# Kernel tuning notes

Measured on AMD Instinct MI355X. Metric: run time of the kernel, lower is better.

Reference implementation:

```python
import jax, jax.numpy as jnp
import numpy as np

B = 2048   # num_trajectories
T = 32     # rollout
I = 1024   # input_size
H = 1024   # hidden_size


def setup_inputs() -> dict:
    key = jax.random.key(0)
    ks = jax.random.split(key, 5)
    head_output = jax.random.normal(ks[0], (B * T, I), jnp.float32)
    rnn_states = jax.random.normal(ks[1], (B, 2 * H), jnp.float32)
    dones = (jax.random.uniform(ks[2], (B * T,)) < 0.05).astype(jnp.float32)
    s = 1.0 / np.sqrt(H)
    w_ih = jax.random.uniform(ks[3], (4 * H, I), jnp.float32, -s, s)
    w_hh = jax.random.uniform(ks[4], (4 * H, H), jnp.float32, -s, s)
    b_ih = jnp.zeros((4 * H,), jnp.float32)  # initialize() fills biases with 0
    b_hh = jnp.zeros((4 * H,), jnp.float32)
    return {"head_output": head_output, "rnn_states": rnn_states, "dones": dones,
            "w_ih": w_ih, "w_hh": w_hh, "b_ih": b_ih, "b_hh": b_hh, "rollout": T}


def reference(head_output, rnn_states, dones, w_ih, w_hh, b_ih, b_hh, rollout):
    # is_seq=True path, n_rnn_layer=1
    n_traj = head_output.shape[0] // rollout
    Hh = rnn_states.shape[1] // 2
    h0, c0 = rnn_states[:, :Hh], rnn_states[:, Hh:]          # [B,H] each
    x = head_output.reshape(n_traj, rollout, -1).transpose(1, 0, 2)  # [T,B,I]
    # is_new_episode = roll(dones, 1, time); first step never resets
    resets = jnp.roll(dones.reshape(n_traj, rollout), 1, axis=1).at[:, 0].set(0.0).T  # [T,B]
    # Precompute the input GEMM for all timesteps in one big matmul
    x_gates = jnp.einsum('tbi,gi->tbg', x, w_ih) + b_ih + b_hh  # [T,B,4H]

    def step(carry, inp):
        h, c = carry
        xg, r = inp
        keep = (1.0 - r)[:, None]
        h = h * keep
        c = c * keep
        gates = xg + h @ w_hh.T                                # [B,4H]
        i, f, g, o = jnp.split(gates, 4, axis=1)               # torch gate order i,f,g,o
        i = jax.nn.sigmoid(i)
        f = jax.nn.sigmoid(f)
        g = jnp.tanh(g)
        o = jax.nn.sigmoid(o)
        c = f * c + i * g
        h = o * jnp.tanh(c)
        return (h, c), h

    (h, c), outs = jax.lax.scan(step, (h0, c0), (x_gates, resets))
    x_out = outs.transpose(1, 0, 2).reshape(n_traj * rollout, -1)  # permute(1,0,2).flatten(0,1)
    new_rnn_states = jnp.concatenate([h, c], axis=1)               # [B,2H]
    return x_out, new_rnn_states
```

## Files before the change

### kernel.cpp

```cpp
#include <hip/hip_runtime.h>
#include <stdint.h>

typedef __attribute__((ext_vector_type(8))) short short8;
typedef __attribute__((ext_vector_type(4))) float f32x4;

#define NTRAJ 2048
#define TSTEP 32
#define HDIM  1024
#define KCAT  2048
#define NGATE 4096

__device__ __forceinline__ unsigned short f2bf(float f) {
  union { float f; unsigned int u; } v; v.f = f;
  unsigned int u = v.u + 0x7FFFu + ((v.u >> 16) & 1u);
  return (unsigned short)(u >> 16);
}
__device__ __forceinline__ float sigmoidf_(float x) {
  return 1.0f / (1.0f + __expf(-x));
}
__device__ __forceinline__ float tanhf_(float x) {
  return 1.0f - 2.0f / (__expf(2.0f * x) + 1.0f);
}

__device__ __forceinline__ void async_lds16(const void* g, void* l) {
  __builtin_amdgcn_global_load_lds(
      (const __attribute__((address_space(1))) unsigned int*)g,
      (__attribute__((address_space(3))) unsigned int*)l, 16, 0, 0);
}


__global__ void cvt_bf16_kernel(const float* __restrict__ src,
                                unsigned short* __restrict__ dst, int n4) {
  int i = blockIdx.x * blockDim.x + threadIdx.x;
  if (i >= n4) return;
  float4 v = ((const float4*)src)[i];
  int e = i * 4;
  int row = e >> 10;
  int col = e & 1023;
  int traj = row >> 5, tt = row & 31;
  size_t de = (((size_t)tt * 2048 + traj) << 10) + col;
  ushort4 o;
  o.x = f2bf(v.x); o.y = f2bf(v.y); o.z = f2bf(v.z); o.w = f2bf(v.w);
  *(ushort4*)&dst[de] = o;
}

__global__ void wcat_kernel(const float* __restrict__ wih,
                            const float* __restrict__ whh,
                            unsigned short* __restrict__ wcat) {
  int i = blockIdx.x * blockDim.x + threadIdx.x;
  int e = i * 4;
  int row = e >> 11;
  int col = e & 2047;
  const float* src = (col < 1024) ? (wih + (size_t)row * 1024 + col)
                                  : (whh + (size_t)row * 1024 + (col - 1024));
  float4 v = *(const float4*)src;
  ushort4 o;
  o.x = f2bf(v.x); o.y = f2bf(v.y); o.z = f2bf(v.z); o.w = f2bf(v.w);
  ((ushort4*)wcat)[i] = o;
}

__global__ void state_prep(const float* __restrict__ rnn,
                           const float* __restrict__ bih,
                           const float* __restrict__ bhh,
                           unsigned short* __restrict__ h0,
                           float* __restrict__ c0,
                           float* __restrict__ bias) {
  int i = blockIdx.x * blockDim.x + threadIdx.x;
  int b = i >> 10, j = i & 1023;
  float hv = rnn[(size_t)b * 2048 + j];
  float cv = rnn[(size_t)b * 2048 + 1024 + j];
  h0[i] = f2bf(hv);
  c0[i] = cv;
  if (i < 4096) bias[i] = bih[i] + bhh[i];
}

__global__ __launch_bounds__(256, 2)
void lstm_step(const unsigned short* __restrict__ X,
               const unsigned short* __restrict__ Wcat,
               const float* __restrict__ bias,
               const float* __restrict__ dones,
               const unsigned short* __restrict__ h_in,
               unsigned short* __restrict__ h_out,
               float* __restrict__ cbuf,
               float* __restrict__ out,
               float* __restrict__ rnn_out,
               int t) {
  __shared__ __align__(16) unsigned short Atile[64 * 32];
  __shared__ __align__(16) unsigned short Btile[4 * 64 * 32];

  const int tid  = threadIdx.x;
  const int wave = tid >> 6;
  const int lane = tid & 63;
  const int l16  = lane & 15;
  const int quad = lane >> 4;

  const int sbid = blockIdx.x;
  const int xcd  = sbid & 7;
  const int ii   = sbid >> 3;
  const int by   = (xcd << 1) | (ii >> 5);
  const int bx   = ii & 31;
  const int bBase = bx * 64;
  const int n0    = by * 64;

  const int col = n0 + wave * 16 + l16;

  f32x4 acc[4][4];
#pragma unroll
  for (int g = 0; g < 4; ++g) {
    float bv = bias[g * 1024 + col];
    f32x4 b4 = {bv, bv, bv, bv};
#pragma unroll
    for (int mt = 0; mt < 4; ++mt) acc[mt][g] = b4;
  }

  const int lr = lane >> 2;
  const int lc = (lane & 3) * 8;
  const unsigned short* aX =
      X + (((size_t)t * 2048) + bBase + wave * 16 + lr) * 1024 + lc;
  const unsigned short* aH =
      h_in + (size_t)(bBase + wave * 16 + lr) * 1024 + lc;
  unsigned short* aD = &Atile[wave * 512];

  const unsigned short* bS[4];
  unsigned short* bD[4];
#pragma unroll
  for (int q = 0; q < 4; ++q) {
    int cb = wave + 4 * q;
    int g  = cb >> 2;
    int row = g * 1024 + n0 + (cb & 3) * 16 + lr;
    bS[q] = Wcat + (size_t)row * 2048 + lc;
    bD[q] = &Btile[cb * 512];
  }

  auto kstep = [&](const unsigned short*& asrc) {
    async_lds16(asrc, aD);
#pragma unroll
    for (int q = 0; q < 4; ++q) async_lds16(bS[q], bD[q]);
    __syncthreads();

    short8 fa[4], fb[4];
#pragma unroll
    for (int mt = 0; mt < 4; ++mt)
      fa[mt] = *(const short8*)&Atile[(mt * 16 + l16) * 32 + quad * 8];
#pragma unroll
    for (int g = 0; g < 4; ++g)
      fb[g] = *(const short8*)&Btile[(g * 64 + wave * 16 + l16) * 32 + quad * 8];
#pragma unroll
    for (int mt = 0; mt < 4; ++mt)
#pragma unroll
      for (int g = 0; g < 4; ++g)
        acc[mt][g] = __builtin_amdgcn_mfma_f32_16x16x32_bf16(fa[mt], fb[g],
                                                             acc[mt][g], 0, 0, 0);
    __syncthreads();

    asrc += 32;
#pragma unroll
    for (int q = 0; q < 4; ++q) bS[q] += 32;
  };

  for (int kk = 0; kk < 32; ++kk) kstep(aX);
  for (int kk = 0; kk < 32; ++kk) kstep(aH);

#pragma unroll
  for (int mt = 0; mt < 4; ++mt) {
#pragma unroll
    for (int v = 0; v < 4; ++v) {
      int b = bBase + mt * 16 + quad * 4 + v;
      float gi = sigmoidf_(acc[mt][0][v]);
      float gf = sigmoidf_(acc[mt][1][v]);
      float gg = tanhf_  (acc[mt][2][v]);
      float go = sigmoidf_(acc[mt][3][v]);
      float cold = cbuf[(size_t)b * 1024 + col];
      float cn = gf * cold + gi * gg;
      float hn = go * tanhf_(cn);
      out[((size_t)b * 32 + t) * 1024 + col] = hn;
      float keep = (t < 31) ? (1.0f - dones[b * 32 + t]) : 1.0f;
      cbuf[(size_t)b * 1024 + col] = cn * keep;
      h_out[(size_t)b * 1024 + col] = f2bf(hn * keep);
      if (t == 31) {
        rnn_out[(size_t)b * 2048 + col] = hn;
        rnn_out[(size_t)b * 2048 + 1024 + col] = cn;
      }
    }
  }
}

extern "C" void kernel_launch(void* const* d_in, const int* in_sizes, int n_in,
                              void* d_out, int out_size, void* d_ws, size_t ws_size,
                              hipStream_t stream) {
  (void)in_sizes; (void)n_in; (void)out_size; (void)ws_size;
  const float* head  = (const float*)d_in[0];
  const float* rnn   = (const float*)d_in[1];
  const float* dones = (const float*)d_in[2];
  const float* wih   = (const float*)d_in[3];
  const float* whh   = (const float*)d_in[4];
  const float* bih   = (const float*)d_in[5];
  const float* bhh   = (const float*)d_in[6];
  float* out = (float*)d_out;
  float* rnn_out = out + (size_t)65536 * 1024;

  char* ws = (char*)d_ws;
  unsigned short* X    = (unsigned short*)(ws);
  unsigned short* Wcat = (unsigned short*)(ws + 134217728);
  float*          bias = (float*)(ws + 150994944);
  unsigned short* h0   = (unsigned short*)(ws + 151011328);
  unsigned short* h1   = (unsigned short*)(ws + 155205632);
  float*          cbuf = (float*)(ws + 159399936);

  cvt_bf16_kernel<<<65536, 256, 0, stream>>>(head, X, 16777216);
  wcat_kernel<<<8192, 256, 0, stream>>>(wih, whh, Wcat);
  state_prep<<<8192, 256, 0, stream>>>(rnn, bih, bhh, h0, cbuf, bias);

  unsigned short* hb[2] = {h0, h1};
  for (int t = 0; t < TSTEP; ++t) {
    lstm_step<<<512, 256, 0, stream>>>(
        X, Wcat, bias, dones, hb[t & 1], hb[(t + 1) & 1], cbuf, out, rnn_out, t);
  }
}
```

Baseline: 2.655 ms.

## Double-buffer LDS tiles and XOR-swizzle layout in LSTM step GEMM

Replaces the single-buffered load-sync-compute-sync K loop with a two-stage LDS ping-pong, so the async global-to-LDS load for the next K slice is issued before the MFMAs on the current one. This also halves the barriers per iteration. It adds an XOR swizzle on the 16-byte column chunk, applied to the global source address and to the LDS read index, to reduce bank conflicts on fragment reads. LDS use doubles, which could limit occupancy at 2 blocks per CU, and the single barrier per step has to cover both the read-after-write and the write-after-read hazards.

```diff
diff --git a/kernel.cpp b/kernel.cpp
--- a/kernel.cpp
+++ b/kernel.cpp
@@ -85,8 +85,8 @@
                float* __restrict__ out,
                float* __restrict__ rnn_out,
                int t) {
-  __shared__ __align__(16) unsigned short Atile[64 * 32];
-  __shared__ __align__(16) unsigned short Btile[4 * 64 * 32];
+  __shared__ __align__(16) unsigned short Ab[2][64 * 32];
+  __shared__ __align__(16) unsigned short Bb[2][4 * 64 * 32];
 
   const int tid  = threadIdx.x;
   const int wave = tid >> 6;
@@ -104,6 +104,8 @@
 
   const int col = n0 + wave * 16 + l16;
 
+  const int sq = quad ^ ((l16 >> 1) & 3);
+
   f32x4 acc[4][4];
 #pragma unroll
   for (int g = 0; g < 4; ++g) {
@@ -114,52 +116,55 @@
   }
 
   const int lr = lane >> 2;
-  const int lc = (lane & 3) * 8;
+  const int lc = ((lane & 3) ^ ((lr >> 1) & 3)) * 8;
   const unsigned short* aX =
       X + (((size_t)t * 2048) + bBase + wave * 16 + lr) * 1024 + lc;
   const unsigned short* aH =
       h_in + (size_t)(bBase + wave * 16 + lr) * 1024 + lc;
-  unsigned short* aD = &Atile[wave * 512];
 
   const unsigned short* bS[4];
-  unsigned short* bD[4];
 #pragma unroll
   for (int q = 0; q < 4; ++q) {
     int cb = wave + 4 * q;
     int g  = cb >> 2;
     int row = g * 1024 + n0 + (cb & 3) * 16 + lr;
     bS[q] = Wcat + (size_t)row * 2048 + lc;
-    bD[q] = &Btile[cb * 512];
-  }
-
-  auto kstep = [&](const unsigned short*& asrc) {
-    async_lds16(asrc, aD);
-#pragma unroll
-    for (int q = 0; q < 4; ++q) async_lds16(bS[q], bD[q]);
-    __syncthreads();
-
+  }
+
+  auto stage = [&](int j, int b) {
+    const unsigned short* as =
+        (j < 32) ? (aX + (size_t)j * 32) : (aH + (size_t)(j - 32) * 32);
+    async_lds16(as, &Ab[b][wave * 512]);
+#pragma unroll
+    for (int q = 0; q < 4; ++q)
+      async_lds16(bS[q] + (size_t)j * 32, &Bb[b][(wave + 4 * q) * 512]);
+  };
+
+  auto compute = [&](int b) {
     short8 fa[4], fb[4];
 #pragma unroll
     for (int mt = 0; mt < 4; ++mt)
-      fa[mt] = *(const short8*)&Atile[(mt * 16 + l16) * 32 + quad * 8];
+      fa[mt] = *(const short8*)&Ab[b][mt * 512 + l16 * 32 + sq * 8];
 #pragma unroll
     for (int g = 0; g < 4; ++g)
-      fb[g] = *(const short8*)&Btile[(g * 64 + wave * 16 + l16) * 32 + quad * 8];
+      fb[g] = *(const short8*)&Bb[b][(g * 4 + wave) * 512 + l16 * 32 + sq * 8];
 #pragma unroll
     for (int mt = 0; mt < 4; ++mt)
 #pragma unroll
       for (int g = 0; g < 4; ++g)
         acc[mt][g] = __builtin_amdgcn_mfma_f32_16x16x32_bf16(fa[mt], fb[g],
                                                              acc[mt][g], 0, 0, 0);
+  };
+
+  stage(0, 0);
+  __syncthreads();
+
+  for (int j = 0; j < 64; ++j) {
+    const int cur = j & 1;
+    if (j < 63) stage(j + 1, cur ^ 1);
+    compute(cur);
     __syncthreads();
-
-    asrc += 32;
-#pragma unroll
-    for (int q = 0; q < 4; ++q) bS[q] += 32;
-  };
-
-  for (int kk = 0; kk < 32; ++kk) kstep(aX);
-  for (int kk = 0; kk < 32; ++kk) kstep(aH);
+  }
 
 #pragma unroll
   for (int mt = 0; mt < 4; ++mt) {
```

Result: no change. 2.681 ms (+1.0%).
